# Optimization experiments

Measured on AMD Instinct MI355X. Metric: run time of the kernel, lower is better.

The kernel has to match this reference:

```python
import jax, jax.numpy as jnp
import numpy as np

F = 64  # dim_features
DIM_TASK = 32


def setup_inputs() -> dict:
    key = jax.random.key(0)
    ks = jax.random.split(key, 16)
    n_state, n_task, n_actor = 65536, 32768, 32768
    E_st, E_ta = 2_000_000, 1_000_000
    inp = {
        'x_state': jax.random.normal(ks[0], (n_state, F), jnp.float32),
        'x_task': jax.random.normal(ks[1], (n_task, F), jnp.float32),
        'x_actor': jax.random.normal(ks[2], (n_actor, F), jnp.float32),
        'edge_attr': jax.random.normal(ks[3], (E_st, 2), jnp.float32),
        # GINEConv edge linear: Linear(2 -> F)
        'We': jax.random.normal(ks[4], (2, F), jnp.float32) * 0.5,
        'be': jnp.zeros((F,), jnp.float32),
        # GinStandardMLP: Linear(F,F) -> ReLU -> Linear(F,F)
        'W1a': jax.random.normal(ks[5], (F, F), jnp.float32) / np.sqrt(F),
        'b1a': jnp.zeros((F,), jnp.float32),
        'W1b': jax.random.normal(ks[6], (F, F), jnp.float32) / np.sqrt(F),
        'b1b': jnp.zeros((F,), jnp.float32),
        # UnactivatedMLP: Linear(F,F) -> ReLU -> Linear(F,1)
        'W2a': jax.random.normal(ks[7], (F, F), jnp.float32) / np.sqrt(F),
        'b2a': jnp.zeros((F,), jnp.float32),
        'W2b': jax.random.normal(ks[8], (F, 1), jnp.float32) / np.sqrt(F),
        'b2b': jnp.zeros((1,), jnp.float32),
        'src_st': jax.random.randint(ks[9], (E_st,), 0, n_state, jnp.int32),
        'dst_st': jax.random.randint(ks[10], (E_st,), 0, n_task, jnp.int32),
        'src_ta': jax.random.randint(ks[11], (E_ta,), 0, n_task, jnp.int32),
        'dst_ta': jax.random.randint(ks[12], (E_ta,), 0, n_actor, jnp.int32),
    }
    return inp


def reference(x_state, x_task, x_actor, edge_attr, We, be, W1a, b1a, W1b, b1b,
              W2a, b2a, W2b, b2b, src_st, dst_st, src_ta, dst_ta):
    n_task = x_task.shape[0]
    n_actor = x_actor.shape[0]
    # --- GINEConv (eps=0): agg_i = sum_e relu(x_src[e] + lin(edge_attr[e])) ---
    msg = jax.nn.relu(x_state[src_st] + edge_attr @ We + be)  # [E_st, F]
    agg = jax.ops.segment_sum(msg, dst_st, num_segments=n_task)  # [n_task, F]
    h = x_task + agg  # (1+eps)*x_r + agg, eps=0
    # GinStandardMLP: Linear-ReLU-Linear
    x1 = jax.nn.relu(h @ W1a + b1a) @ W1b + b1b  # [n_task, F]
    # --- GINConv (eps=0): agg2_i = sum_e x1[src[e]] ---
    agg2 = jax.ops.segment_sum(x1[src_ta], dst_ta, num_segments=n_actor)  # [n_actor, F]
    h2 = x_actor + agg2
    # UnactivatedMLP: Linear-ReLU-Linear -> 1
    logits = jax.nn.relu(h2 @ W2a + b2a) @ W2b + b2b  # [n_actor, 1]
    return logits.reshape(-1, DIM_TASK)
```

## Files before the change

kernel.cpp:

```cpp
#include <hip/hip_runtime.h>

#define F 64
#define TILE 8192
#define NB 1024
#define ROWSB 32
#define CAP1 2560
#define CAP2 1408

typedef __attribute__((ext_vector_type(8))) short bf8;
typedef __attribute__((ext_vector_type(4))) float f4;
typedef __attribute__((ext_vector_type(2))) float fl2;

__device__ __forceinline__ unsigned short f2bf(float f) {
    unsigned u = __float_as_uint(f);
    unsigned r = u + 0x7fffu + ((u >> 16) & 1u);
    return (unsigned short)(r >> 16);
}
__device__ __forceinline__ float bf2f(unsigned short h) {
    return __uint_as_float((unsigned)h << 16);
}
__device__ __forceinline__ fl2 unpack2(unsigned d) {
    fl2 r;
    r.x = __uint_as_float(d << 16);
    r.y = __uint_as_float(d & 0xffff0000u);
    return r;
}

__device__ __forceinline__ int block_scan_1024(int c, int tid, int* scratch) {
    int lane = tid & 63, wv = tid >> 6;
    int s = c;
    #pragma unroll
    for (int off = 1; off < 64; off <<= 1) {
        int u = __shfl_up(s, off);
        if (lane >= off) s += u;
    }
    if (lane == 63) scratch[wv] = s;
    __syncthreads();
    if (tid < 64) {
        int ws = (tid < 16) ? scratch[tid] : 0;
        int t = ws;
        #pragma unroll
        for (int off = 1; off < 16; off <<= 1) {
            int u = __shfl_up(t, off);
            if (tid >= off) t += u;
        }
        if (tid < 16) scratch[16 + tid] = t - ws;
    }
    __syncthreads();
    return s - c + scratch[16 + wv];
}

__global__ __launch_bounds__(1024) void prep_kernel(
    const float4* __restrict__ xs4, ushort4* __restrict__ xsb4, int n4,
    const int* __restrict__ src1, const int* __restrict__ dst1,
    const float* __restrict__ ea, int E1,
    int* __restrict__ cur1, uint2* __restrict__ keyA1,
    const int* __restrict__ src2, const int* __restrict__ dst2, int E2,
    int* __restrict__ cur2, unsigned* __restrict__ keyA2,
    int nBin1, int nBin2)
{
    __shared__ uint2 stage[TILE];
    __shared__ int hist[NB], lcur[NB], comb[NB];
    __shared__ int scratch[32];
    int bid = blockIdx.x;
    int tid = threadIdx.x;

    if (bid < nBin1) {
        int base = bid * TILE;
        int cnt = min(TILE, E1 - base);
        hist[tid] = 0;
        __syncthreads();
        int myb[8]; unsigned msd[8], mpk[8];
        #pragma unroll
        for (int j = 0; j < 8; ++j) {
            int idx = tid + 1024 * j;
            if (idx < cnt) {
                int d = dst1[base + idx];
                int s = src1[base + idx];
                float2 e2 = ((const float2* __restrict__)ea)[base + idx];
                myb[j] = d >> 5;
                msd[j] = ((unsigned)s << 16) | (unsigned)d;
                mpk[j] = ((unsigned)f2bf(e2.y) << 16) | (unsigned)f2bf(e2.x);
                atomicAdd(&hist[myb[j]], 1);
            } else myb[j] = -1;
        }
        __syncthreads();
        int c = hist[tid];
        int gb = CAP1 * tid + atomicAdd(&cur1[tid], c);
        int excl = block_scan_1024(c, tid, scratch);
        comb[tid] = gb - excl;
        lcur[tid] = excl;
        __syncthreads();
        #pragma unroll
        for (int j = 0; j < 8; ++j) {
            if (myb[j] >= 0) {
                int p = atomicAdd(&lcur[myb[j]], 1);
                stage[p] = make_uint2(msd[j], mpk[j]);
            }
        }
        __syncthreads();
        #pragma unroll
        for (int j = 0; j < 8; ++j) {
            int p = tid + 1024 * j;
            if (p < cnt) {
                uint2 f = stage[p];
                int b = (int)(f.x & 0xffffu) >> 5;
                keyA1[comb[b] + p] = f;
            }
        }
        return;
    }

    if (bid < nBin1 + nBin2) {
        unsigned* ustage = (unsigned*)stage;
        int base = (bid - nBin1) * TILE;
        int cnt = min(TILE, E2 - base);
        hist[tid] = 0;
        __syncthreads();
        int myb[8]; unsigned msd[8];
        #pragma unroll
        for (int j = 0; j < 8; ++j) {
            int idx = tid + 1024 * j;
            if (idx < cnt) {
                int d = dst2[base + idx];
                int s = src2[base + idx];
                myb[j] = d >> 5;
                msd[j] = ((unsigned)s << 16) | (unsigned)d;
                atomicAdd(&hist[myb[j]], 1);
            } else myb[j] = -1;
        }
        __syncthreads();
        int c = hist[tid];
        int gb = CAP2 * tid + atomicAdd(&cur2[tid], c);
        int excl = block_scan_1024(c, tid, scratch);
        comb[tid] = gb - excl;
        lcur[tid] = excl;
        __syncthreads();
        #pragma unroll
        for (int j = 0; j < 8; ++j) {
            if (myb[j] >= 0) {
                int p = atomicAdd(&lcur[myb[j]], 1);
                ustage[p] = msd[j];
            }
        }
        __syncthreads();
        #pragma unroll
        for (int j = 0; j < 8; ++j) {
            int p = tid + 1024 * j;
            if (p < cnt) {
                unsigned f = ustage[p];
                int b = (int)(f & 0xffffu) >> 5;
                keyA2[comb[b] + p] = f;
            }
        }
        return;
    }

    {
        int i = (bid - nBin1 - nBin2) * 1024 + tid;
        if (i < n4) {
            float4 v = xs4[i];
            ushort4 o;
            o.x = f2bf(v.x); o.y = f2bf(v.y); o.z = f2bf(v.z); o.w = f2bf(v.w);
            xsb4[i] = o;
        }
    }
}

__global__ __launch_bounds__(512) void sg1_kernel(
    const uint2* __restrict__ keyA,
    const ushort* __restrict__ xsb,
    const float* __restrict__ x_task,
    const float* __restrict__ We, const float* __restrict__ be,
    const int* __restrict__ gcursor,
    float* __restrict__ hout, int n)
{
    __shared__ uint2 lpay[CAP1];
    __shared__ int hh[ROWSB], rst[ROWSB], cur[ROWSB];
    int tid = threadIdx.x;
    int b = blockIdx.x;
    int cnt = min(gcursor[b], CAP1);
    const uint2* ka = keyA + (size_t)b * CAP1;

    uint2 myk[5];
    #pragma unroll
    for (int j = 0; j < 5; ++j) {
        int idx = tid + 512 * j;
        if (idx < cnt) myk[j] = ka[idx];
    }
    if (tid < ROWSB) hh[tid] = 0;
    __syncthreads();
    #pragma unroll
    for (int j = 0; j < 5; ++j) {
        int idx = tid + 512 * j;
        if (idx < cnt) atomicAdd(&hh[myk[j].x & 31u], 1);
    }
    __syncthreads();
    if (tid < 64) {
        int cc = (tid < ROWSB) ? hh[tid] : 0;
        int s = cc;
        #pragma unroll
        for (int off = 1; off < ROWSB; off <<= 1) {
            int u = __shfl_up(s, off);
            if (tid >= off) s += u;
        }
        if (tid < ROWSB) { rst[tid] = s - cc; cur[tid] = s - cc; }
    }
    __syncthreads();
    #pragma unroll
    for (int j = 0; j < 5; ++j) {
        int idx = tid + 512 * j;
        if (idx < cnt) {
            int p = atomicAdd(&cur[myk[j].x & 31u], 1);
            lpay[p] = myk[j];
        }
    }
    __syncthreads();

    int wave = tid >> 6, lane = tid & 63;
    int q = lane & 7, g = lane >> 3;
    int gid = (wave << 3) | g;
    int r   = gid >> 1;
    int h   = gid & 1;
    int row = b * ROWSB + r;

    fl2 w0p[4], w1p[4], bbp[4];
    {
        float4 a0 = ((const float4* __restrict__)We)[q * 2];
        float4 a1 = ((const float4* __restrict__)We)[q * 2 + 1];
        float4 c0 = ((const float4* __restrict__)(We + F))[q * 2];
        float4 c1 = ((const float4* __restrict__)(We + F))[q * 2 + 1];
        float4 d0 = ((const float4* __restrict__)be)[q * 2];
        float4 d1 = ((const float4* __restrict__)be)[q * 2 + 1];
        w0p[0] = (fl2){a0.x, a0.y}; w0p[1] = (fl2){a0.z, a0.w};
        w0p[2] = (fl2){a1.x, a1.y}; w0p[3] = (fl2){a1.z, a1.w};
        w1p[0] = (fl2){c0.x, c0.y}; w1p[1] = (fl2){c0.z, c0.w};
        w1p[2] = (fl2){c1.x, c1.y}; w1p[3] = (fl2){c1.z, c1.w};
        bbp[0] = (fl2){d0.x, d0.y}; bbp[1] = (fl2){d0.z, d0.w};
        bbp[2] = (fl2){d1.x, d1.y}; bbp[3] = (fl2){d1.z, d1.w};
    }
    const fl2 zero2 = {0.f, 0.f};

    int c  = hh[r];
    int m0 = (c + 1) >> 1;
    int sh = rst[r] + (h ? m0 : 0);
    int m  = h ? (c - m0) : m0;

    fl2 acc2[4];
    #pragma unroll
    for (int p = 0; p < 4; ++p) acc2[p] = zero2;

    unsigned pk0 = 0, pk1 = 0, pk2 = 0, pk3 = 0;
    uint4 xw0 = {0,0,0,0}, xw1 = {0,0,0,0}, xw2 = {0,0,0,0}, xw3 = {0,0,0,0};

    #define SG1_LOAD(J, K)                                                          \
    if ((K) < m) {                                                                  \
        uint2 t = lpay[sh + (K)];                                                   \
        pk##J = t.y;                                                                \
        xw##J = ((const uint4* __restrict__)(xsb + ((size_t)(t.x >> 16) << 6)))[q]; \
    }

    #define SG1_COMP(PK, XW)                                                        \
    {                                                                               \
        fl2 ex = {__uint_as_float((PK) << 16), __uint_as_float((PK) << 16)};        \
        fl2 ey = {__uint_as_float((PK) & 0xffff0000u),                              \
                  __uint_as_float((PK) & 0xffff0000u)};                             \
        fl2 cc, t2;                                                                 \
        cc = __builtin_elementwise_fma(ey, w1p[0], bbp[0]);                         \
        cc = __builtin_elementwise_fma(ex, w0p[0], cc);                             \
        t2 = unpack2((XW).x) + cc;                                                  \
        acc2[0] += __builtin_elementwise_max(t2, zero2);                            \
        cc = __builtin_elementwise_fma(ey, w1p[1], bbp[1]);                         \
        cc = __builtin_elementwise_fma(ex, w0p[1], cc);                             \
        t2 = unpack2((XW).y) + cc;                                                  \
        acc2[1] += __builtin_elementwise_max(t2, zero2);                            \
        cc = __builtin_elementwise_fma(ey, w1p[2], bbp[2]);                         \
        cc = __builtin_elementwise_fma(ex, w0p[2], cc);                             \
        t2 = unpack2((XW).z) + cc;                                                  \
        acc2[2] += __builtin_elementwise_max(t2, zero2);                            \
        cc = __builtin_elementwise_fma(ey, w1p[3], bbp[3]);                         \
        cc = __builtin_elementwise_fma(ex, w0p[3], cc);                             \
        t2 = unpack2((XW).w) + cc;                                                  \
        acc2[3] += __builtin_elementwise_max(t2, zero2);                            \
    }

    SG1_LOAD(0, 0)
    SG1_LOAD(1, 1)
    SG1_LOAD(2, 2)
    SG1_LOAD(3, 3)
    int i = 0;
    for (; i + 4 <= m; i += 4) {
        SG1_COMP(pk0, xw0) SG1_LOAD(0, i + 4)
        SG1_COMP(pk1, xw1) SG1_LOAD(1, i + 5)
        SG1_COMP(pk2, xw2) SG1_LOAD(2, i + 6)
        SG1_COMP(pk3, xw3) SG1_LOAD(3, i + 7)
    }
    if (i < m)     SG1_COMP(pk0, xw0)
    if (i + 1 < m) SG1_COMP(pk1, xw1)
    if (i + 2 < m) SG1_COMP(pk2, xw2)
    #undef SG1_LOAD
    #undef SG1_COMP

    float acc[8];
    #pragma unroll
    for (int p = 0; p < 4; ++p) { acc[2 * p] = acc2[p].x; acc[2 * p + 1] = acc2[p].y; }
    #pragma unroll
    for (int j = 0; j < 8; ++j) acc[j] += __shfl_xor(acc[j], 8);

    if (h == 0 && row < n) {
        const float4* xt = (const float4* __restrict__)(x_task + (size_t)row * F + q * 8);
        float4 t0 = xt[0], t1 = xt[1];
        float4 o0, o1;
        o0.x = acc[0] + t0.x; o0.y = acc[1] + t0.y; o0.z = acc[2] + t0.z; o0.w = acc[3] + t0.w;
        o1.x = acc[4] + t1.x; o1.y = acc[5] + t1.y; o1.z = acc[6] + t1.z; o1.w = acc[7] + t1.w;
        float4* hp = (float4*)(hout + (size_t)row * F + q * 8);
        hp[0] = o0; hp[1] = o1;
    }
}

__global__ __launch_bounds__(256) void mlp1_kernel(
    const float* __restrict__ hin,
    const float* __restrict__ W1a, const float* __restrict__ b1a,
    const float* __restrict__ W1b, const float* __restrict__ b1b,
    ushort* __restrict__ x1b, int n)
{
    __shared__ float ldsH[4][16 * 68];
    int tid = threadIdx.x;
    int wave = tid >> 6, lane = tid & 63;
    int quad = lane >> 4, col = lane & 15;
    int rowbase = blockIdx.x * 64 + wave * 16;
    if (rowbase >= n) return;
    float* ltile = ldsH[wave];

    bf8 Wah[2][4], Wal[2][4], Wbh[2][4], Wbl[2][4];
    float ba1[4], bb1[4];
    #pragma unroll
    for (int kh = 0; kh < 2; ++kh)
        #pragma unroll
        for (int c = 0; c < 4; ++c) {
            bf8 th, tl, sh, sl;
            #pragma unroll
            for (int j = 0; j < 8; ++j) {
                int k = kh * 32 + quad * 8 + j;
                float wa = W1a[k * F + c * 16 + col];
                unsigned short h1 = f2bf(wa);
                th[j] = (short)h1; tl[j] = (short)f2bf(wa - bf2f(h1));
                float wb = W1b[k * F + c * 16 + col];
                unsigned short h2 = f2bf(wb);
                sh[j] = (short)h2; sl[j] = (short)f2bf(wb - bf2f(h2));
            }
            Wah[kh][c] = th; Wal[kh][c] = tl;
            Wbh[kh][c] = sh; Wbl[kh][c] = sl;
        }
    #pragma unroll
    for (int c = 0; c < 4; ++c) { ba1[c] = b1a[c * 16 + col]; bb1[c] = b1b[c * 16 + col]; }

    const float* hrow = hin + (size_t)(rowbase + col) * F + quad * 8;
    bf8 Ah[2], Al[2];
    #pragma unroll
    for (int kh = 0; kh < 2; ++kh) {
        bf8 th, tl;
        #pragma unroll
        for (int j = 0; j < 8; ++j) {
            float a = hrow[kh * 32 + j];
            unsigned short h1 = f2bf(a);
            th[j] = (short)h1; tl[j] = (short)f2bf(a - bf2f(h1));
        }
        Ah[kh] = th; Al[kh] = tl;
    }

    #pragma unroll
    for (int c = 0; c < 4; ++c) {
        f4 acc = {0.f, 0.f, 0.f, 0.f};
        #pragma unroll
        for (int kh = 0; kh < 2; ++kh) {
            acc = __builtin_amdgcn_mfma_f32_16x16x32_bf16(Ah[kh], Wah[kh][c], acc, 0, 0, 0);
            acc = __builtin_amdgcn_mfma_f32_16x16x32_bf16(Ah[kh], Wal[kh][c], acc, 0, 0, 0);
            acc = __builtin_amdgcn_mfma_f32_16x16x32_bf16(Al[kh], Wah[kh][c], acc, 0, 0, 0);
        }
        #pragma unroll
        for (int r = 0; r < 4; ++r)
            ltile[(quad * 4 + r) * 68 + c * 16 + col] = fmaxf(acc[r] + ba1[c], 0.f);
    }
    bf8 A2h[2], A2l[2];
    #pragma unroll
    for (int kh = 0; kh < 2; ++kh) {
        bf8 th, tl;
        #pragma unroll
        for (int j = 0; j < 8; ++j) {
            float a = ltile[col * 68 + kh * 32 + quad * 8 + j];
            unsigned short h1 = f2bf(a);
            th[j] = (short)h1; tl[j] = (short)f2bf(a - bf2f(h1));
        }
        A2h[kh] = th; A2l[kh] = tl;
    }
    #pragma unroll
    for (int c = 0; c < 4; ++c) {
        f4 acc = {0.f, 0.f, 0.f, 0.f};
        #pragma unroll
        for (int kh = 0; kh < 2; ++kh) {
            acc = __builtin_amdgcn_mfma_f32_16x16x32_bf16(A2h[kh], Wbh[kh][c], acc, 0, 0, 0);
            acc = __builtin_amdgcn_mfma_f32_16x16x32_bf16(A2h[kh], Wbl[kh][c], acc, 0, 0, 0);
            acc = __builtin_amdgcn_mfma_f32_16x16x32_bf16(A2l[kh], Wbh[kh][c], acc, 0, 0, 0);
        }
        #pragma unroll
        for (int r = 0; r < 4; ++r)
            ltile[(quad * 4 + r) * 68 + c * 16 + col] = acc[r] + bb1[c];
    }
    int rr = lane >> 2, cc = (lane & 3) * 16;
    unsigned o[8];
    #pragma unroll
    for (int j = 0; j < 8; ++j) {
        unsigned lo = f2bf(ltile[rr * 68 + cc + 2 * j]);
        unsigned hi = f2bf(ltile[rr * 68 + cc + 2 * j + 1]);
        o[j] = lo | (hi << 16);
    }
    uint4* dst = (uint4*)(x1b + (size_t)(rowbase + rr) * F + cc);
    dst[0] = make_uint4(o[0], o[1], o[2], o[3]);
    dst[1] = make_uint4(o[4], o[5], o[6], o[7]);
}

__global__ __launch_bounds__(512) void sg2_kernel(
    const unsigned* __restrict__ keyA,
    const ushort* __restrict__ x1b,
    const float* __restrict__ x_actor,
    const int* __restrict__ gcursor,
    float* __restrict__ h2out, int n)
{
    __shared__ unsigned lpay[CAP2];
    __shared__ int hh[ROWSB], rst[ROWSB], cur[ROWSB];
    int tid = threadIdx.x;
    int b = blockIdx.x;
    int cnt = min(gcursor[b], CAP2);
    const unsigned* ka = keyA + (size_t)b * CAP2;

    unsigned myk[3];
    #pragma unroll
    for (int j = 0; j < 3; ++j) {
        int idx = tid + 512 * j;
        if (idx < cnt) myk[j] = ka[idx];
    }
    if (tid < ROWSB) hh[tid] = 0;
    __syncthreads();
    #pragma unroll
    for (int j = 0; j < 3; ++j) {
        int idx = tid + 512 * j;
        if (idx < cnt) atomicAdd(&hh[myk[j] & 31u], 1);
    }
    __syncthreads();
    if (tid < 64) {
        int cc = (tid < ROWSB) ? hh[tid] : 0;
        int s = cc;
        #pragma unroll
        for (int off = 1; off < ROWSB; off <<= 1) {
            int u = __shfl_up(s, off);
            if (tid >= off) s += u;
        }
        if (tid < ROWSB) { rst[tid] = s - cc; cur[tid] = s - cc; }
    }
    __syncthreads();
    #pragma unroll
    for (int j = 0; j < 3; ++j) {
        int idx = tid + 512 * j;
        if (idx < cnt) {
            int p = atomicAdd(&cur[myk[j] & 31u], 1);
            lpay[p] = myk[j];
        }
    }
    __syncthreads();

    int wave = tid >> 6, lane = tid & 63;
    int q = lane & 7, g = lane >> 3;
    int gid = (wave << 3) | g;
    int r   = gid >> 1;
    int h   = gid & 1;
    int row = b * ROWSB + r;
    const fl2 zero2 = {0.f, 0.f};

    int c  = hh[r];
    int m0 = (c + 1) >> 1;
    int sh = rst[r] + (h ? m0 : 0);
    int m  = h ? (c - m0) : m0;

    fl2 acc2[4];
    #pragma unroll
    for (int p = 0; p < 4; ++p) acc2[p] = zero2;

    uint4 xw0 = {0,0,0,0}, xw1 = {0,0,0,0}, xw2 = {0,0,0,0}, xw3 = {0,0,0,0};

    #define SG2_LOAD(J, K)                                                          \
    if ((K) < m) {                                                                  \
        unsigned t = lpay[sh + (K)];                                                \
        xw##J = ((const uint4* __restrict__)(x1b + ((size_t)(t >> 16) << 6)))[q];   \
    }

    #define SG2_COMP(XW)                                                            \
    {                                                                               \
        acc2[0] += unpack2((XW).x);                                                 \
        acc2[1] += unpack2((XW).y);                                                 \
        acc2[2] += unpack2((XW).z);                                                 \
        acc2[3] += unpack2((XW).w);                                                 \
    }

    SG2_LOAD(0, 0)
    SG2_LOAD(1, 1)
    SG2_LOAD(2, 2)
    SG2_LOAD(3, 3)
    int i = 0;
    for (; i + 4 <= m; i += 4) {
        SG2_COMP(xw0) SG2_LOAD(0, i + 4)
        SG2_COMP(xw1) SG2_LOAD(1, i + 5)
        SG2_COMP(xw2) SG2_LOAD(2, i + 6)
        SG2_COMP(xw3) SG2_LOAD(3, i + 7)
    }
    if (i < m)     SG2_COMP(xw0)
    if (i + 1 < m) SG2_COMP(xw1)
    if (i + 2 < m) SG2_COMP(xw2)
    #undef SG2_LOAD
    #undef SG2_COMP

    float acc[8];
    #pragma unroll
    for (int p = 0; p < 4; ++p) { acc[2 * p] = acc2[p].x; acc[2 * p + 1] = acc2[p].y; }
    #pragma unroll
    for (int j = 0; j < 8; ++j) acc[j] += __shfl_xor(acc[j], 8);

    if (h == 0 && row < n) {
        const float4* xt = (const float4* __restrict__)(x_actor + (size_t)row * F + q * 8);
        float4 t0 = xt[0], t1 = xt[1];
        float4 o0, o1;
        o0.x = acc[0] + t0.x; o0.y = acc[1] + t0.y; o0.z = acc[2] + t0.z; o0.w = acc[3] + t0.w;
        o1.x = acc[4] + t1.x; o1.y = acc[5] + t1.y; o1.z = acc[6] + t1.z; o1.w = acc[7] + t1.w;
        float4* hp = (float4*)(h2out + (size_t)row * F + q * 8);
        hp[0] = o0; hp[1] = o1;
    }
}

__global__ __launch_bounds__(256) void mlp2_kernel(
    const float* __restrict__ h2in,
    const float* __restrict__ W2a, const float* __restrict__ b2a,
    const float* __restrict__ W2b, const float* __restrict__ b2b,
    float* __restrict__ out, int n)
{
    int tid = threadIdx.x;
    int wave = tid >> 6, lane = tid & 63;
    int quad = lane >> 4, col = lane & 15;
    int rowbase = blockIdx.x * 64 + wave * 16;
    if (rowbase >= n) return;

    bf8 Wah[2][4], Wal[2][4];
    float ba1[4], wo[4];
    #pragma unroll
    for (int kh = 0; kh < 2; ++kh)
        #pragma unroll
        for (int c = 0; c < 4; ++c) {
            bf8 th, tl;
            #pragma unroll
            for (int j = 0; j < 8; ++j) {
                int k = kh * 32 + quad * 8 + j;
                float w = W2a[k * F + c * 16 + col];
                unsigned short h1 = f2bf(w);
                th[j] = (short)h1; tl[j] = (short)f2bf(w - bf2f(h1));
            }
            Wah[kh][c] = th; Wal[kh][c] = tl;
        }
    #pragma unroll
    for (int c = 0; c < 4; ++c) { ba1[c] = b2a[c * 16 + col]; wo[c] = W2b[c * 16 + col]; }
    float bias2 = b2b[0];

    const float* hrow = h2in + (size_t)(rowbase + col) * F + quad * 8;
    bf8 Ah[2], Al[2];
    #pragma unroll
    for (int kh = 0; kh < 2; ++kh) {
        bf8 th, tl;
        #pragma unroll
        for (int j = 0; j < 8; ++j) {
            float a = hrow[kh * 32 + j];
            unsigned short h1 = f2bf(a);
            th[j] = (short)h1; tl[j] = (short)f2bf(a - bf2f(h1));
        }
        Ah[kh] = th; Al[kh] = tl;
    }

    float partial[4] = {0.f, 0.f, 0.f, 0.f};
    #pragma unroll
    for (int c = 0; c < 4; ++c) {
        f4 acc = {0.f, 0.f, 0.f, 0.f};
        #pragma unroll
        for (int kh = 0; kh < 2; ++kh) {
            acc = __builtin_amdgcn_mfma_f32_16x16x32_bf16(Ah[kh], Wah[kh][c], acc, 0, 0, 0);
            acc = __builtin_amdgcn_mfma_f32_16x16x32_bf16(Ah[kh], Wal[kh][c], acc, 0, 0, 0);
            acc = __builtin_amdgcn_mfma_f32_16x16x32_bf16(Al[kh], Wah[kh][c], acc, 0, 0, 0);
        }
        #pragma unroll
        for (int r = 0; r < 4; ++r)
            partial[r] += fmaxf(acc[r] + ba1[c], 0.f) * wo[c];
    }
    #pragma unroll
    for (int off = 1; off < 16; off <<= 1)
        #pragma unroll
        for (int r = 0; r < 4; ++r)
            partial[r] += __shfl_xor(partial[r], off);
    if (col == 0) {
        #pragma unroll
        for (int r = 0; r < 4; ++r)
            out[rowbase + quad * 4 + r] = partial[r] + bias2;
    }
}

extern "C" void kernel_launch(void* const* d_in, const int* in_sizes, int n_in,
                              void* d_out, int out_size, void* d_ws, size_t ws_size,
                              hipStream_t stream)
{
    const float* x_state   = (const float*)d_in[0];
    const float* x_task    = (const float*)d_in[1];
    const float* x_actor   = (const float*)d_in[2];
    const float* edge_attr = (const float*)d_in[3];
    const float* We        = (const float*)d_in[4];
    const float* be        = (const float*)d_in[5];
    const float* W1a       = (const float*)d_in[6];
    const float* b1a       = (const float*)d_in[7];
    const float* W1b       = (const float*)d_in[8];
    const float* b1b       = (const float*)d_in[9];
    const float* W2a       = (const float*)d_in[10];
    const float* b2a       = (const float*)d_in[11];
    const float* W2b       = (const float*)d_in[12];
    const float* b2b       = (const float*)d_in[13];
    const int*   src_st    = (const int*)d_in[14];
    const int*   dst_st    = (const int*)d_in[15];
    const int*   src_ta    = (const int*)d_in[16];
    const int*   dst_ta    = (const int*)d_in[17];

    int n_state = in_sizes[0] / F;
    int n_task  = in_sizes[1] / F;
    int n_actor = in_sizes[2] / F;
    int E_st    = in_sizes[14];
    int E_ta    = in_sizes[16];

    ushort*   x1b   = (ushort*)d_ws;
    float*    hbig  = (float*)(x1b + (size_t)n_task * F);
    ushort*   xsb   = (ushort*)(hbig + (size_t)n_task * F);
    uint2*    keyA1 = (uint2*)(xsb + (size_t)n_state * F);
    unsigned* keyA2 = (unsigned*)(keyA1 + (size_t)NB * CAP1);
    int*      cur1  = (int*)(keyA2 + (size_t)NB * CAP2);
    int*      cur2  = cur1 + NB;

    int n4    = n_state * F / 4;
    int nCvt  = (n4 + 1023) / 1024;
    int nBin1 = (E_st + TILE - 1) / TILE;
    int nBin2 = (E_ta + TILE - 1) / TILE;

    hipMemsetAsync(cur1, 0, 2 * NB * sizeof(int), stream);
    prep_kernel<<<nBin1 + nBin2 + nCvt, 1024, 0, stream>>>(
        (const float4*)x_state, (ushort4*)xsb, n4,
        src_st, dst_st, edge_attr, E_st, cur1, keyA1,
        src_ta, dst_ta, E_ta, cur2, keyA2,
        nBin1, nBin2);
    sg1_kernel<<<NB, 512, 0, stream>>>(
        keyA1, xsb, x_task, We, be, cur1, hbig, n_task);
    mlp1_kernel<<<(n_task + 63) / 64, 256, 0, stream>>>(
        hbig, W1a, b1a, W1b, b1b, x1b, n_task);
    sg2_kernel<<<NB, 512, 0, stream>>>(
        keyA2, x1b, x_actor, cur2, hbig, n_actor);
    mlp2_kernel<<<(n_actor + 63) / 64, 256, 0, stream>>>(
        hbig, W2a, b2a, W2b, b2b, (float*)d_out, n_actor);
}
```

Baseline: 203.1 us.

## Fuse MLPs into segment-gather kernels and prepack MFMA weights once

Removes the separate mlp1 and mlp2 kernels. Each gather block now stages its 32 aggregated rows in LDS, and two waves run the split-bf16 MFMA MLP on that tile, writing x1 or the logits directly. The weights are converted once into a packed hi/lo bf16 layout by an extra block in the prep kernel, so the MLP waves no longer rebuild them per block. This drops two launches, the fp32 h round trip through global memory and the repeated weight conversion. The cost is that only 2 of 8 waves do the MLP while the others sit idle, LDS use per block grows, and the gather kernels' tails get longer.

```diff
diff --git a/kernel.cpp b/kernel.cpp
--- a/kernel.cpp
+++ b/kernel.cpp
@@ -6,6 +6,14 @@
 #define ROWSB 32
 #define CAP1 2560
 #define CAP2 1408
+#define HS 68
+
+#define WP1AH 0
+#define WP1AL 4096
+#define WP1BH 8192
+#define WP1BL 12288
+#define WP2AH 16384
+#define WP2AL 20480
 
 typedef __attribute__((ext_vector_type(8))) short bf8;
 typedef __attribute__((ext_vector_type(4))) float f4;
@@ -57,6 +65,8 @@
     int* __restrict__ cur1, uint2* __restrict__ keyA1,
     const int* __restrict__ src2, const int* __restrict__ dst2, int E2,
     int* __restrict__ cur2, unsigned* __restrict__ keyA2,
+    const float* __restrict__ W1a, const float* __restrict__ W1b,
+    const float* __restrict__ W2a, ushort* __restrict__ wp,
     int nBin1, int nBin2)
 {
     __shared__ uint2 stage[TILE];
@@ -65,8 +75,35 @@
     int bid = blockIdx.x;
     int tid = threadIdx.x;
 
-    if (bid < nBin1) {
-        int base = bid * TILE;
+    if (bid == 0) {
+        int fid = tid & 511;
+        int col = fid & 15, quad = (fid >> 4) & 3, c = (fid >> 6) & 3, kh = (fid >> 8) & 1;
+        const float* Wsrc = (tid < 512) ? W1a : W1b;
+        ushort* dh = wp + ((tid < 512) ? WP1AH : WP1BH);
+        ushort* dl = wp + ((tid < 512) ? WP1AL : WP1BL);
+        #pragma unroll
+        for (int j = 0; j < 8; ++j) {
+            int k = kh * 32 + quad * 8 + j;
+            float w = Wsrc[k * F + c * 16 + col];
+            unsigned short hi = f2bf(w);
+            dh[fid * 8 + j] = hi;
+            dl[fid * 8 + j] = f2bf(w - bf2f(hi));
+        }
+        if (tid < 512) {
+            #pragma unroll
+            for (int j = 0; j < 8; ++j) {
+                int k = kh * 32 + quad * 8 + j;
+                float w = W2a[k * F + c * 16 + col];
+                unsigned short hi = f2bf(w);
+                wp[WP2AH + fid * 8 + j] = hi;
+                wp[WP2AL + fid * 8 + j] = f2bf(w - bf2f(hi));
+            }
+        }
+        return;
+    }
+
+    if (bid <= nBin1) {
+        int base = (bid - 1) * TILE;
         int cnt = min(TILE, E1 - base);
         hist[tid] = 0;
         __syncthreads();
@@ -111,9 +148,9 @@
         return;
     }
 
-    if (bid < nBin1 + nBin2) {
+    if (bid <= nBin1 + nBin2) {
         unsigned* ustage = (unsigned*)stage;
-        int base = (bid - nBin1) * TILE;
+        int base = (bid - 1 - nBin1) * TILE;
         int cnt = min(TILE, E2 - base);
         hist[tid] = 0;
         __syncthreads();
@@ -157,7 +194,7 @@
     }
 
     {
-        int i = (bid - nBin1 - nBin2) * 1024 + tid;
+        int i = (bid - 1 - nBin1 - nBin2) * 1024 + tid;
         if (i < n4) {
             float4 v = xs4[i];
             ushort4 o;
@@ -173,10 +210,14 @@
     const float* __restrict__ x_task,
     const float* __restrict__ We, const float* __restrict__ be,
     const int* __restrict__ gcursor,
-    float* __restrict__ hout, int n)
+    const ushort* __restrict__ wp,
+    const float* __restrict__ b1a, const float* __restrict__ b1b,
+    ushort* __restrict__ x1b, int n)
 {
     __shared__ uint2 lpay[CAP1];
     __shared__ int hh[ROWSB], rst[ROWSB], cur[ROWSB];
+    __shared__ float htile[ROWSB * HS];
+    __shared__ float ltile[2 * 16 * HS];
     int tid = threadIdx.x;
     int b = blockIdx.x;
     int cnt = min(gcursor[b], CAP1);
@@ -313,111 +354,96 @@
         float4 o0, o1;
         o0.x = acc[0] + t0.x; o0.y = acc[1] + t0.y; o0.z = acc[2] + t0.z; o0.w = acc[3] + t0.w;
         o1.x = acc[4] + t1.x; o1.y = acc[5] + t1.y; o1.z = acc[6] + t1.z; o1.w = acc[7] + t1.w;
-        float4* hp = (float4*)(hout + (size_t)row * F + q * 8);
+        float4* hp = (float4*)&htile[r * HS + q * 8];
         hp[0] = o0; hp[1] = o1;
     }
-}
-
-__global__ __launch_bounds__(256) void mlp1_kernel(
-    const float* __restrict__ hin,
-    const float* __restrict__ W1a, const float* __restrict__ b1a,
-    const float* __restrict__ W1b, const float* __restrict__ b1b,
-    ushort* __restrict__ x1b, int n)
-{
-    __shared__ float ldsH[4][16 * 68];
-    int tid = threadIdx.x;
-    int wave = tid >> 6, lane = tid & 63;
-    int quad = lane >> 4, col = lane & 15;
-    int rowbase = blockIdx.x * 64 + wave * 16;
-    if (rowbase >= n) return;
-    float* ltile = ldsH[wave];
-
-    bf8 Wah[2][4], Wal[2][4], Wbh[2][4], Wbl[2][4];
-    float ba1[4], bb1[4];
-    #pragma unroll
-    for (int kh = 0; kh < 2; ++kh)
-        #pragma unroll
-        for (int c = 0; c < 4; ++c) {
-            bf8 th, tl, sh, sl;
+    __syncthreads();
+
+    if (wave < 2) {
+        int t = wave;
+        int quad = lane >> 4, col = lane & 15;
+        float* lt = ltile + t * 16 * HS;
+
+        bf8 Ah[2], Al[2];
+        #pragma unroll
+        for (int kh = 0; kh < 2; ++kh) {
+            const float4* hr4 = (const float4*)&htile[(t * 16 + col) * HS + kh * 32 + quad * 8];
+            float4 v0 = hr4[0], v1 = hr4[1];
+            float av[8] = {v0.x, v0.y, v0.z, v0.w, v1.x, v1.y, v1.z, v1.w};
+            bf8 th, tl;
             #pragma unroll
             for (int j = 0; j < 8; ++j) {
-                int k = kh * 32 + quad * 8 + j;
-                float wa = W1a[k * F + c * 16 + col];
-                unsigned short h1 = f2bf(wa);
-                th[j] = (short)h1; tl[j] = (short)f2bf(wa - bf2f(h1));
-                float wb = W1b[k * F + c * 16 + col];
-                unsigned short h2 = f2bf(wb);
-                sh[j] = (short)h2; sl[j] = (short)f2bf(wb - bf2f(h2));
-            }
-            Wah[kh][c] = th; Wal[kh][c] = tl;
-            Wbh[kh][c] = sh; Wbl[kh][c] = sl;
-        }
-    #pragma unroll
-    for (int c = 0; c < 4; ++c) { ba1[c] = b1a[c * 16 + col]; bb1[c] = b1b[c * 16 + col]; }
-
-    const float* hrow = hin + (size_t)(rowbase + col) * F + quad * 8;
-    bf8 Ah[2], Al[2];
-    #pragma unroll
-    for (int kh = 0; kh < 2; ++kh) {
-        bf8 th, tl;
-        #pragma unroll
-        for (int j = 0; j < 8; ++j) {
-            float a = hrow[kh * 32 + j];
-            unsigned short h1 = f2bf(a);
-            th[j] = (short)h1; tl[j] = (short)f2bf(a - bf2f(h1));
-        }
-        Ah[kh] = th; Al[kh] = tl;
-    }
-
-    #pragma unroll
-    for (int c = 0; c < 4; ++c) {
-        f4 acc = {0.f, 0.f, 0.f, 0.f};
+                unsigned short h1 = f2bf(av[j]);
+                th[j] = (short)h1; tl[j] = (short)f2bf(av[j] - bf2f(h1));
+            }
+            Ah[kh] = th; Al[kh] = tl;
+        }
+        #pragma unroll
+        for (int c4i = 0; c4i < 4; ++c4i) {
+            int f0 = ((0 * 4 + c4i) * 4 + quad) * 16 + col;
+            int f1 = ((1 * 4 + c4i) * 4 + quad) * 16 + col;
+            bf8 wh0 = *(const bf8*)(wp + WP1AH + f0 * 8);
+            bf8 wl0 = *(const bf8*)(wp + WP1AL + f0 * 8);
+            bf8 wh1 = *(const bf8*)(wp + WP1AH + f1 * 8);
+            bf8 wl1 = *(const bf8*)(wp + WP1AL + f1 * 8);
+            f4 accm = {0.f, 0.f, 0.f, 0.f};
+            accm = __builtin_amdgcn_mfma_f32_16x16x32_bf16(Ah[0], wh0, accm, 0, 0, 0);
+            accm = __builtin_amdgcn_mfma_f32_16x16x32_bf16(Ah[0], wl0, accm, 0, 0, 0);
+            accm = __builtin_amdgcn_mfma_f32_16x16x32_bf16(Al[0], wh0, accm, 0, 0, 0);
+            accm = __builtin_amdgcn_mfma_f32_16x16x32_bf16(Ah[1], wh1, accm, 0, 0, 0);
+            accm = __builtin_amdgcn_mfma_f32_16x16x32_bf16(Ah[1], wl1, accm, 0, 0, 0);
+            accm = __builtin_amdgcn_mfma_f32_16x16x32_bf16(Al[1], wh1, accm, 0, 0, 0);
+            float ba = b1a[c4i * 16 + col];
+            #pragma unroll
+            for (int rr = 0; rr < 4; ++rr)
+                lt[(quad * 4 + rr) * HS + c4i * 16 + col] = fmaxf(accm[rr] + ba, 0.f);
+        }
+        bf8 A2h[2], A2l[2];
         #pragma unroll
         for (int kh = 0; kh < 2; ++kh) {
-            acc = __builtin_amdgcn_mfma_f32_16x16x32_bf16(Ah[kh], Wah[kh][c], acc, 0, 0, 0);
-            acc = __builtin_amdgcn_mfma_f32_16x16x32_bf16(Ah[kh], Wal[kh][c], acc, 0, 0, 0);
-            acc = __builtin_amdgcn_mfma_f32_16x16x32_bf16(Al[kh], Wah[kh][c], acc, 0, 0, 0);
-        }
-        #pragma unroll
-        for (int r = 0; r < 4; ++r)
-            ltile[(quad * 4 + r) * 68 + c * 16 + col] = fmaxf(acc[r] + ba1[c], 0.f);
-    }
-    bf8 A2h[2], A2l[2];
-    #pragma unroll
-    for (int kh = 0; kh < 2; ++kh) {
-        bf8 th, tl;
-        #pragma unroll
-        for (int j = 0; j < 8; ++j) {
-            float a = ltile[col * 68 + kh * 32 + quad * 8 + j];
-            unsigned short h1 = f2bf(a);
-            th[j] = (short)h1; tl[j] = (short)f2bf(a - bf2f(h1));
-        }
-        A2h[kh] = th; A2l[kh] = tl;
-    }
-    #pragma unroll
-    for (int c = 0; c < 4; ++c) {
-        f4 acc = {0.f, 0.f, 0.f, 0.f};
-        #pragma unroll
-        for (int kh = 0; kh < 2; ++kh) {
-            acc = __builtin_amdgcn_mfma_f32_16x16x32_bf16(A2h[kh], Wbh[kh][c], acc, 0, 0, 0);
-            acc = __builtin_amdgcn_mfma_f32_16x16x32_bf16(A2h[kh], Wbl[kh][c], acc, 0, 0, 0);
-            acc = __builtin_amdgcn_mfma_f32_16x16x32_bf16(A2l[kh], Wbh[kh][c], acc, 0, 0, 0);
-        }
-        #pragma unroll
-        for (int r = 0; r < 4; ++r)
-            ltile[(quad * 4 + r) * 68 + c * 16 + col] = acc[r] + bb1[c];
-    }
-    int rr = lane >> 2, cc = (lane & 3) * 16;
-    unsigned o[8];
-    #pragma unroll
-    for (int j = 0; j < 8; ++j) {
-        unsigned lo = f2bf(ltile[rr * 68 + cc + 2 * j]);
-        unsigned hi = f2bf(ltile[rr * 68 + cc + 2 * j + 1]);
-        o[j] = lo | (hi << 16);
-    }
-    uint4* dst = (uint4*)(x1b + (size_t)(rowbase + rr) * F + cc);
-    dst[0] = make_uint4(o[0], o[1], o[2], o[3]);
-    dst[1] = make_uint4(o[4], o[5], o[6], o[7]);
+            const float4* lr4 = (const float4*)&lt[col * HS + kh * 32 + quad * 8];
+            float4 v0 = lr4[0], v1 = lr4[1];
+            float av[8] = {v0.x, v0.y, v0.z, v0.w, v1.x, v1.y, v1.z, v1.w};
+            bf8 th, tl;
+            #pragma unroll
+            for (int j = 0; j < 8; ++j) {
+                unsigned short h1 = f2bf(av[j]);
+                th[j] = (short)h1; tl[j] = (short)f2bf(av[j] - bf2f(h1));
+            }
+            A2h[kh] = th; A2l[kh] = tl;
+        }
+        #pragma unroll
+        for (int c4i = 0; c4i < 4; ++c4i) {
+            int f0 = ((0 * 4 + c4i) * 4 + quad) * 16 + col;
+            int f1 = ((1 * 4 + c4i) * 4 + quad) * 16 + col;
+            bf8 wh0 = *(const bf8*)(wp + WP1BH + f0 * 8);
+            bf8 wl0 = *(const bf8*)(wp + WP1BL + f0 * 8);
+            bf8 wh1 = *(const bf8*)(wp + WP1BH + f1 * 8);
+            bf8 wl1 = *(const bf8*)(wp + WP1BL + f1 * 8);
+            f4 accm = {0.f, 0.f, 0.f, 0.f};
+            accm = __builtin_amdgcn_mfma_f32_16x16x32_bf16(A2h[0], wh0, accm, 0, 0, 0);
+            accm = __builtin_amdgcn_mfma_f32_16x16x32_bf16(A2h[0], wl0, accm, 0, 0, 0);
+            accm = __builtin_amdgcn_mfma_f32_16x16x32_bf16(A2l[0], wh0, accm, 0, 0, 0);
+            accm = __builtin_amdgcn_mfma_f32_16x16x32_bf16(A2h[1], wh1, accm, 0, 0, 0);
+            accm = __builtin_amdgcn_mfma_f32_16x16x32_bf16(A2h[1], wl1, accm, 0, 0, 0);
+            accm = __builtin_amdgcn_mfma_f32_16x16x32_bf16(A2l[1], wh1, accm, 0, 0, 0);
+            float bb = b1b[c4i * 16 + col];
+            #pragma unroll
+            for (int rr = 0; rr < 4; ++rr)
+                lt[(quad * 4 + rr) * HS + c4i * 16 + col] = accm[rr] + bb;
+        }
+        int rr = lane >> 2, cc2 = (lane & 3) * 16;
+        unsigned o[8];
+        #pragma unroll
+        for (int j = 0; j < 8; ++j) {
+            unsigned lo = f2bf(lt[rr * HS + cc2 + 2 * j]);
+            unsigned hi = f2bf(lt[rr * HS + cc2 + 2 * j + 1]);
+            o[j] = lo | (hi << 16);
+        }
+        uint4* dst = (uint4*)(x1b + (size_t)(b * ROWSB + t * 16 + rr) * F + cc2);
+        dst[0] = make_uint4(o[0], o[1], o[2], o[3]);
+        dst[1] = make_uint4(o[4], o[5], o[6], o[7]);
+    }
 }
 
 __global__ __launch_bounds__(512) void sg2_kernel(
@@ -425,10 +451,14 @@
     const ushort* __restrict__ x1b,
     const float* __restrict__ x_actor,
     const int* __restrict__ gcursor,
-    float* __restrict__ h2out, int n)
+    const ushort* __restrict__ wp,
+    const float* __restrict__ b2a, const float* __restrict__ W2b,
+    const float* __restrict__ b2b,
+    float* __restrict__ out, int n)
 {
     __shared__ unsigned lpay[CAP2];
     __shared__ int hh[ROWSB], rst[ROWSB], cur[ROWSB];
+    __shared__ float htile[ROWSB * HS];
     int tid = threadIdx.x;
     int b = blockIdx.x;
     int cnt = min(gcursor[b], CAP2);
@@ -531,80 +561,63 @@
         float4 o0, o1;
         o0.x = acc[0] + t0.x; o0.y = acc[1] + t0.y; o0.z = acc[2] + t0.z; o0.w = acc[3] + t0.w;
         o1.x = acc[4] + t1.x; o1.y = acc[5] + t1.y; o1.z = acc[6] + t1.z; o1.w = acc[7] + t1.w;
-        float4* hp = (float4*)(h2out + (size_t)row * F + q * 8);
+        float4* hp = (float4*)&htile[r * HS + q * 8];
         hp[0] = o0; hp[1] = o1;
     }
-}
-
-__global__ __launch_bounds__(256) void mlp2_kernel(
-    const float* __restrict__ h2in,
-    const float* __restrict__ W2a, const float* __restrict__ b2a,
-    const float* __restrict__ W2b, const float* __restrict__ b2b,
-    float* __restrict__ out, int n)
-{
-    int tid = threadIdx.x;
-    int wave = tid >> 6, lane = tid & 63;
-    int quad = lane >> 4, col = lane & 15;
-    int rowbase = blockIdx.x * 64 + wave * 16;
-    if (rowbase >= n) return;
-
-    bf8 Wah[2][4], Wal[2][4];
-    float ba1[4], wo[4];
-    #pragma unroll
-    for (int kh = 0; kh < 2; ++kh)
-        #pragma unroll
-        for (int c = 0; c < 4; ++c) {
+    __syncthreads();
+
+    if (wave < 2) {
+        int t = wave;
+        int quad = lane >> 4, col = lane & 15;
+
+        bf8 Ah[2], Al[2];
+        #pragma unroll
+        for (int kh = 0; kh < 2; ++kh) {
+            const float4* hr4 = (const float4*)&htile[(t * 16 + col) * HS + kh * 32 + quad * 8];
+            float4 v0 = hr4[0], v1 = hr4[1];
+            float av[8] = {v0.x, v0.y, v0.z, v0.w, v1.x, v1.y, v1.z, v1.w};
             bf8 th, tl;
             #pragma unroll
             for (int j = 0; j < 8; ++j) {
-                int k = kh * 32 + quad * 8 + j;
-                float w = W2a[k * F + c * 16 + col];
-                unsigned short h1 = f2bf(w);
-                th[j] = (short)h1; tl[j] = (short)f2bf(w - bf2f(h1));
-            }
-            Wah[kh][c] = th; Wal[kh][c] = tl;
-        }
-    #pragma unroll
-    for (int c = 0; c < 4; ++c) { ba1[c] = b2a[c * 16 + col]; wo[c] = W2b[c * 16 + col]; }
-    float bias2 = b2b[0];
-
-    const float* hrow = h2in + (size_t)(rowbase + col) * F + quad * 8;
-    bf8 Ah[2], Al[2];
-    #pragma unroll
-    for (int kh = 0; kh < 2; ++kh) {
-        bf8 th, tl;
-        #pragma unroll
-        for (int j = 0; j < 8; ++j) {
-            float a = hrow[kh * 32 + j];
-            unsigned short h1 = f2bf(a);
-            th[j] = (short)h1; tl[j] = (short)f2bf(a - bf2f(h1));
-        }
-        Ah[kh] = th; Al[kh] = tl;
-    }
-
-    float partial[4] = {0.f, 0.f, 0.f, 0.f};
-    #pragma unroll
-    for (int c = 0; c < 4; ++c) {
-        f4 acc = {0.f, 0.f, 0.f, 0.f};
-        #pragma unroll
-        for (int kh = 0; kh < 2; ++kh) {
-            acc = __builtin_amdgcn_mfma_f32_16x16x32_bf16(Ah[kh], Wah[kh][c], acc, 0, 0, 0);
-            acc = __builtin_amdgcn_mfma_f32_16x16x32_bf16(Ah[kh], Wal[kh][c], acc, 0, 0, 0);
-            acc = __builtin_amdgcn_mfma_f32_16x16x32_bf16(Al[kh], Wah[kh][c], acc, 0, 0, 0);
-        }
-        #pragma unroll
-        for (int r = 0; r < 4; ++r)
-            partial[r] += fmaxf(acc[r] + ba1[c], 0.f) * wo[c];
-    }
-    #pragma unroll
-    for (int off = 1; off < 16; off <<= 1)
-        #pragma unroll
-        for (int r = 0; r < 4; ++r)
-            partial[r] += __shfl_xor(partial[r], off);
-    if (col == 0) {
-        #pragma unroll
-        for (int r = 0; r < 4; ++r)
-            out[rowbase + quad * 4 + r] = partial[r] + bias2;
+                unsigned short h1 = f2bf(av[j]);
+                th[j] = (short)h1; tl[j] = (short)f2bf(av[j] - bf2f(h1));
+            }
+            Ah[kh] = th; Al[kh] = tl;
+        }
+
+        float partial[4] = {0.f, 0.f, 0.f, 0.f};
+        #pragma unroll
+        for (int c4i = 0; c4i < 4; ++c4i) {
+            int f0 = ((0 * 4 + c4i) * 4 + quad) * 16 + col;
+            int f1 = ((1 * 4 + c4i) * 4 + quad) * 16 + col;
+            bf8 wh0 = *(const bf8*)(wp + WP2AH + f0 * 8);
+            bf8 wl0 = *(const bf8*)(wp + WP2AL + f0 * 8);
+            bf8 wh1 = *(const bf8*)(wp + WP2AH + f1 * 8);
+            bf8 wl1 = *(const bf8*)(wp + WP2AL + f1 * 8);
+            f4 accm = {0.f, 0.f, 0.f, 0.f};
+            accm = __builtin_amdgcn_mfma_f32_16x16x32_bf16(Ah[0], wh0, accm, 0, 0, 0);
+            accm = __builtin_amdgcn_mfma_f32_16x16x32_bf16(Ah[0], wl0, accm, 0, 0, 0);
+            accm = __builtin_amdgcn_mfma_f32_16x16x32_bf16(Al[0], wh0, accm, 0, 0, 0);
+            accm = __builtin_amdgcn_mfma_f32_16x16x32_bf16(Ah[1], wh1, accm, 0, 0, 0);
+            accm = __builtin_amdgcn_mfma_f32_16x16x32_bf16(Ah[1], wl1, accm, 0, 0, 0);
+            accm = __builtin_amdgcn_mfma_f32_16x16x32_bf16(Al[1], wh1, accm, 0, 0, 0);
+            float ba = b2a[c4i * 16 + col];
+            float w_o = W2b[c4i * 16 + col];
+            #pragma unroll
+            for (int rr = 0; rr < 4; ++rr)
+                partial[rr] += fmaxf(accm[rr] + ba, 0.f) * w_o;
+        }
+        #pragma unroll
+        for (int off = 1; off < 16; off <<= 1)
+            #pragma unroll
+            for (int rr = 0; rr < 4; ++rr)
+                partial[rr] += __shfl_xor(partial[rr], off);
+        if (col == 0) {
+            float bias2 = b2b[0];
+            #pragma unroll
+            for (int rr = 0; rr < 4; ++rr)
+                out[b * ROWSB + t * 16 + quad * 4 + rr] = partial[rr] + bias2;
+        }
     }
 }
 
@@ -639,6 +652,7 @@
 
     ushort*   x1b   = (ushort*)d_ws;
     float*    hbig  = (float*)(x1b + (size_t)n_task * F);
+    ushort*   wp    = (ushort*)hbig;
     ushort*   xsb   = (ushort*)(hbig + (size_t)n_task * F);
     uint2*    keyA1 = (uint2*)(xsb + (size_t)n_state * F);
     unsigned* keyA2 = (unsigned*)(keyA1 + (size_t)NB * CAP1);
@@ -651,17 +665,14 @@
     int nBin2 = (E_ta + TILE - 1) / TILE;
 
     hipMemsetAsync(cur1, 0, 2 * NB * sizeof(int), stream);
-    prep_kernel<<<nBin1 + nBin2 + nCvt, 1024, 0, stream>>>(
+    prep_kernel<<<1 + nBin1 + nBin2 + nCvt, 1024, 0, stream>>>(
         (const float4*)x_state, (ushort4*)xsb, n4,
         src_st, dst_st, edge_attr, E_st, cur1, keyA1,
         src_ta, dst_ta, E_ta, cur2, keyA2,
+        W1a, W1b, W2a, wp,
         nBin1, nBin2);
     sg1_kernel<<<NB, 512, 0, stream>>>(
-        keyA1, xsb, x_task, We, be, cur1, hbig, n_task);
-    mlp1_kernel<<<(n_task + 63) / 64, 256, 0, stream>>>(
-        hbig, W1a, b1a, W1b, b1b, x1b, n_task);
+        keyA1, xsb, x_task, We, be, cur1, wp, b1a, b1b, x1b, n_task);
     sg2_kernel<<<NB, 512, 0, stream>>>(
-        keyA2, x1b, x_actor, cur2, hbig, n_actor);
-    mlp2_kernel<<<(n_actor + 63) / 64, 256, 0, stream>>>(
-        hbig, W2a, b2a, W2b, b2b, (float*)d_out, n_actor);
-}
+        keyA2, x1b, x_actor, cur2, wp, b2a, W2b, b2b, (float*)d_out, n_actor);
+}
```

New measurement: 196.0 us. 1.04x faster.
